# Performance work log

Hardware: AMD Instinct MI355X
Metric: run time of the kernel (lower is better)

The kernel has to match this reference:

```python
import jax, jax.numpy as jnp
import numpy as np

B = 32          # batch_size
M = 1024        # mesh_num (nodes per sub-graph)
D_IN = 128      # sub_node_feature_input_dim
D_OUT = 128     # sub_node_feature_output_dim
E_DIM = 64      # embedding dim per node


def setup_inputs() -> dict:
    key = jax.random.key(0)
    k1, k2, k3, k4 = jax.random.split(key, 4)
    return {
        "node_feature_group": jax.random.normal(k1, (B * M, D_IN), dtype=jnp.float32),
        "embedding_group": jax.random.normal(k2, (B * M, E_DIM), dtype=jnp.float32),
        "W1": jax.random.normal(k3, (D_OUT, D_IN), dtype=jnp.float32) * (1.0 / np.sqrt(D_IN)),
        "W2": jax.random.normal(k4, (D_OUT, D_OUT), dtype=jnp.float32) * (1.0 / np.sqrt(D_OUT)),
    }


def reference(node_feature_group, embedding_group, W1, W2):
    # The torch module builds a (B*M)x(B*M) block-diagonal adjacency via
    # torch.block_diag; off-block entries are exactly zero, and row sums /
    # D^-1/2 A D^-1/2 normalization act per block, so we compute per-graph.
    E = embedding_group.reshape(B, M, E_DIM)
    adj = jnp.maximum(jnp.einsum('bme,bne->bmn', E, E), 0.0)  # clamp(E E^T, 0)
    adj = adj + jnp.eye(M, dtype=adj.dtype)                   # A = adj + I
    d = adj.sum(-1)                                           # [B, M]
    dinv = d ** -0.5                                          # symmetric=True
    dad = dinv[:, :, None] * adj * dinv[:, None, :]           # D^-1/2 A D^-1/2

    X = node_feature_group.reshape(B, M, D_IN)
    y = jax.nn.relu(jnp.einsum('bmn,bnd->bmd', dad, X) @ W1.T)   # gcn1
    y = jax.nn.relu(jnp.einsum('bmn,bnd->bmd', dad, y) @ W2.T)   # gcn2
    # Dropout is identity in eval mode.
    return y.reshape(B * M, D_OUT)
```

## Files before the change

### kernel.cpp

```cpp
#include <hip/hip_runtime.h>
#include <stdint.h>

#define B_  32
#define M_  1024
#define DF  128
#define ED  64

typedef __attribute__((ext_vector_type(8))) short short8;
typedef __attribute__((ext_vector_type(4))) float floatx4;

__device__ inline unsigned short f2bf(float f) {
    union { float f; unsigned u; } v; v.f = f;
    unsigned r = v.u + 0x7fffu + ((v.u >> 16) & 1u);
    return (unsigned short)(r >> 16);
}

__device__ inline void load_lds16(const void* g, void* l) {
    __builtin_amdgcn_global_load_lds(
        (const __attribute__((address_space(1))) unsigned int*)g,
        (__attribute__((address_space(3))) unsigned int*)l, 16, 0, 0);
}

__global__ __launch_bounds__(256) void cast_kernel(
    const float* __restrict__ E, const float* __restrict__ W1,
    const float* __restrict__ W2, unsigned short* __restrict__ Ebf,
    unsigned short* __restrict__ W1bf, unsigned short* __restrict__ W2bf) {
    const int NE = B_ * M_ * ED;
    const int NW = DF * DF;
    int idx = (blockIdx.x * 256 + threadIdx.x) * 4;
    const float* src; unsigned short* dst; int off;
    if (idx < NE)            { src = E;  dst = Ebf;  off = idx; }
    else if (idx < NE + NW)  { src = W1; dst = W1bf; off = idx - NE; }
    else                     { src = W2; dst = W2bf; off = idx - NE - NW; }
    float4 v = *(const float4*)(src + off);
    ushort4 o;
    o.x = f2bf(v.x); o.y = f2bf(v.y); o.z = f2bf(v.z); o.w = f2bf(v.w);
    *(ushort4*)(dst + off) = o;
}

__global__ __launch_bounds__(256) void build_s_kernel(
    const unsigned short* __restrict__ Ebf, unsigned short* __restrict__ S,
    float* __restrict__ dinv) {
    int mt2 = blockIdx.x, b = blockIdx.y;
    int t = threadIdx.x;
    int w = t >> 6, lane = t & 63, quad = lane >> 4, lc = lane & 15;
    __shared__ unsigned short sEn[128][72];
    const unsigned short* Eb = Ebf + (size_t)b * M_ * ED;
    unsigned short* Sg = S + ((size_t)b << 20);
    int base_m = mt2 * 64 + w * 16;

    short8 afr[2];
    for (int ks = 0; ks < 2; ++ks)
        afr[ks] = *(const short8*)(Eb + (size_t)(base_m + lc) * ED + ks * 32 + quad * 8);
    floatx4 rsum = (floatx4){0.f, 0.f, 0.f, 0.f};

    for (int nc = 0; nc < 8; ++nc) {
        __syncthreads();
        for (int it = 0; it < 4; ++it) {
            int c = t + 256 * it;
            int row = c >> 3, off = (c & 7) * 8;
            *(short8*)(&sEn[row][off]) =
                *(const short8*)(Eb + (size_t)(nc * 128 + row) * ED + off);
        }
        __syncthreads();
        for (int nt = 0; nt < 8; ++nt) {
            short8 b0 = *(const short8*)(&sEn[nt * 16 + lc][quad * 8]);
            short8 b1 = *(const short8*)(&sEn[nt * 16 + lc][32 + quad * 8]);
            floatx4 s = (floatx4){0.f, 0.f, 0.f, 0.f};
            s = __builtin_amdgcn_mfma_f32_16x16x32_bf16(afr[0], b0, s, 0, 0, 0);
            s = __builtin_amdgcn_mfma_f32_16x16x32_bf16(afr[1], b1, s, 0, 0, 0);
            int n = nc * 128 + nt * 16 + lc;
            for (int r = 0; r < 4; ++r) {
                int m = base_m + quad * 4 + r;
                float v = fmaxf(s[r], 0.f);
                if (m == n) v += 1.0f;
                rsum[r] += v;
                Sg[(size_t)m * M_ + n] = f2bf(v);
            }
        }
    }
    for (int r = 0; r < 4; ++r) {
        float v = rsum[r];
        v += __shfl_xor(v, 1, 16);
        v += __shfl_xor(v, 2, 16);
        v += __shfl_xor(v, 4, 16);
        v += __shfl_xor(v, 8, 16);
        if (lc == 0)
            dinv[b * M_ + base_m + quad * 4 + r] = rsqrtf(v);
    }
}

__global__ __launch_bounds__(256) void tscale_kernel(
    const float* __restrict__ X, const float* __restrict__ dinv,
    unsigned short* __restrict__ Xt) {
    int nt = blockIdx.x, b = blockIdx.y;
    int t = threadIdx.x;
    __shared__ unsigned short sT[128][72];
    int nloc = t >> 5;
    int d4 = (t & 31) * 4;
    for (int pass = 0; pass < 8; ++pass) {
        int n = pass * 8 + nloc;
        int grow = b * M_ + nt * 64 + n;
        float sc = dinv[grow];
        float4 v = *(const float4*)(X + (size_t)grow * DF + d4);
        sT[d4 + 0][n] = f2bf(v.x * sc);
        sT[d4 + 1][n] = f2bf(v.y * sc);
        sT[d4 + 2][n] = f2bf(v.z * sc);
        sT[d4 + 3][n] = f2bf(v.w * sc);
    }
    __syncthreads();
    for (int it = 0; it < 4; ++it) {
        int c = t + 256 * it;
        int d = c >> 3, off = (c & 7) * 8;
        *(short8*)(Xt + (size_t)(b * DF + d) * M_ + nt * 64 + off) =
            *(const short8*)(&sT[d][off]);
    }
}

template <int MODE>
__global__ __launch_bounds__(256) void gemm_kernel(
    const unsigned short* __restrict__ S,
    const unsigned short* __restrict__ Pt,
    const unsigned short* __restrict__ Wbf,
    const float* __restrict__ dinv,
    unsigned short* __restrict__ OutT,
    float* __restrict__ OutF) {
    int bx = blockIdx.x, b = blockIdx.y;
    int m0 = bx * 64;
    int t = threadIdx.x;
    int w = t >> 6, lane = t & 63, quad = lane >> 4, lc = lane & 15;
    int wr = w & 1, wc = w >> 1;

    __shared__ unsigned short lds[26112];
    unsigned short* sA = lds;
    unsigned short* sB = lds + 4096;
    unsigned short* sY = lds;
    unsigned short* sW = lds + 8704;

    const unsigned short* Sg = S + ((size_t)b << 20);
    const unsigned short* Pb = Pt + (size_t)b * DF * M_;

    floatx4 acc[2][4];
    for (int i = 0; i < 2; ++i)
        for (int j = 0; j < 4; ++j) acc[i][j] = (floatx4){0.f, 0.f, 0.f, 0.f};

    for (int nc = 0; nc < 16; ++nc) {
        __syncthreads();
        for (int r = 0; r < 2; ++r) {
            int te = r * 256 + w * 64 + lane;
            const void* gp = Sg + (size_t)(m0 + (te >> 3)) * M_ + nc * 64 + (te & 7) * 8;
            load_lds16(gp, (char*)sA + (r * 256 + w * 64) * 16);
        }
        for (int r = 0; r < 4; ++r) {
            int te = r * 256 + w * 64 + lane;
            const void* gp = Pb + (size_t)(te >> 3) * M_ + nc * 64 + (te & 7) * 8;
            load_lds16(gp, (char*)sB + (r * 256 + w * 64) * 16);
        }
        __syncthreads();
        for (int ks = 0; ks < 2; ++ks) {
            short8 afr[2], bfr[4];
            for (int i = 0; i < 2; ++i)
                afr[i] = *(const short8*)(&sA[(wr * 32 + i * 16 + lc) * 64 + ks * 32 + quad * 8]);
            for (int j = 0; j < 4; ++j)
                bfr[j] = *(const short8*)(&sB[(wc * 64 + j * 16 + lc) * 64 + ks * 32 + quad * 8]);
            for (int i = 0; i < 2; ++i)
                for (int j = 0; j < 4; ++j)
                    acc[i][j] = __builtin_amdgcn_mfma_f32_16x16x32_bf16(afr[i], bfr[j], acc[i][j], 0, 0, 0);
        }
    }

    float dv[2][4];
    for (int i = 0; i < 2; ++i)
        for (int r = 0; r < 4; ++r)
            dv[i][r] = dinv[b * M_ + m0 + wr * 32 + i * 16 + quad * 4 + r];
    __syncthreads();
    for (int i = 0; i < 2; ++i)
        for (int j = 0; j < 4; ++j) {
            int mrow = wr * 32 + i * 16 + quad * 4;
            int col = wc * 64 + j * 16 + lc;
            for (int r = 0; r < 4; ++r)
                sY[(mrow + r) * 136 + col] = f2bf(acc[i][j][r] * dv[i][r]);
        }
    for (int it = 0; it < 8; ++it) {
        int c = t + 256 * it;
        int row = c >> 4, off = (c & 15) * 8;
        *(short8*)(&sW[row * 136 + off]) = *(const short8*)(Wbf + row * DF + off);
    }
    __syncthreads();
    floatx4 accH[2][4];
    for (int i = 0; i < 2; ++i)
        for (int j = 0; j < 4; ++j) accH[i][j] = (floatx4){0.f, 0.f, 0.f, 0.f};
    for (int ks = 0; ks < 4; ++ks) {
        short8 afr[2], bfr[4];
        for (int i = 0; i < 2; ++i)
            afr[i] = *(const short8*)(&sY[(wr * 32 + i * 16 + lc) * 136 + ks * 32 + quad * 8]);
        for (int j = 0; j < 4; ++j)
            bfr[j] = *(const short8*)(&sW[(wc * 64 + j * 16 + lc) * 136 + ks * 32 + quad * 8]);
        for (int i = 0; i < 2; ++i)
            for (int j = 0; j < 4; ++j)
                accH[i][j] = __builtin_amdgcn_mfma_f32_16x16x32_bf16(afr[i], bfr[j], accH[i][j], 0, 0, 0);
    }
    if (MODE == 2) {
        float* Ob = OutF + ((size_t)b * M_ + m0) * DF;
        for (int i = 0; i < 2; ++i)
            for (int j = 0; j < 4; ++j) {
                int mrow = wr * 32 + i * 16 + quad * 4;
                int col = wc * 64 + j * 16 + lc;
                for (int r = 0; r < 4; ++r)
                    Ob[(size_t)(mrow + r) * DF + col] = fmaxf(accH[i][j][r], 0.f);
            }
    } else {
        __syncthreads();
        unsigned short* sT = sW;
        for (int i = 0; i < 2; ++i)
            for (int j = 0; j < 4; ++j) {
                int mrow = wr * 32 + i * 16 + quad * 4;
                int col = wc * 64 + j * 16 + lc;
                for (int r = 0; r < 4; ++r)
                    sT[col * 72 + mrow + r] = f2bf(fmaxf(accH[i][j][r], 0.f) * dv[i][r]);
            }
        __syncthreads();
        for (int it = 0; it < 4; ++it) {
            int c = t + 256 * it;
            int o = c >> 3, off = (c & 7) * 8;
            *(short8*)(OutT + (size_t)(b * DF + o) * M_ + m0 + off) =
                *(const short8*)(&sT[o * 72 + off]);
        }
    }
}

__global__ __launch_bounds__(256) void degree_kernel(
    const unsigned short* __restrict__ Ebf, float* __restrict__ dinv) {
    int mt = blockIdx.x, b = blockIdx.y;
    int t = threadIdx.x;
    int w = t >> 6, lane = t & 63, quad = lane >> 4, lc = lane & 15;
    __shared__ unsigned short sEn[128][72];
    const unsigned short* Eb = Ebf + (size_t)b * M_ * ED;
    short8 afr[2][2];
    for (int i = 0; i < 2; ++i) {
        int row = mt * 128 + w * 32 + i * 16 + lc;
        for (int ks = 0; ks < 2; ++ks)
            afr[i][ks] = *(const short8*)(Eb + (size_t)row * ED + ks * 32 + quad * 8);
    }
    floatx4 rsum[2];
    rsum[0] = (floatx4){0.f,0.f,0.f,0.f};
    rsum[1] = (floatx4){0.f,0.f,0.f,0.f};
    for (int nc = 0; nc < 8; ++nc) {
        __syncthreads();
        for (int it = 0; it < 4; ++it) {
            int c = t + 256 * it;
            int row = c >> 3, off = (c & 7) * 8;
            *(short8*)(&sEn[row][off]) =
                *(const short8*)(Eb + (size_t)(nc * 128 + row) * ED + off);
        }
        __syncthreads();
        for (int nt = 0; nt < 8; ++nt) {
            short8 b0 = *(const short8*)(&sEn[nt * 16 + lc][quad * 8]);
            short8 b1 = *(const short8*)(&sEn[nt * 16 + lc][32 + quad * 8]);
            for (int i = 0; i < 2; ++i) {
                floatx4 s = (floatx4){0.f,0.f,0.f,0.f};
                s = __builtin_amdgcn_mfma_f32_16x16x32_bf16(afr[i][0], b0, s, 0, 0, 0);
                s = __builtin_amdgcn_mfma_f32_16x16x32_bf16(afr[i][1], b1, s, 0, 0, 0);
                for (int r = 0; r < 4; ++r) rsum[i][r] += fmaxf(s[r], 0.f);
            }
        }
    }
    for (int i = 0; i < 2; ++i)
        for (int r = 0; r < 4; ++r) {
            float v = rsum[i][r];
            v += __shfl_xor(v, 1, 16);
            v += __shfl_xor(v, 2, 16);
            v += __shfl_xor(v, 4, 16);
            v += __shfl_xor(v, 8, 16);
            if (lc == 0) {
                int row = mt * 128 + w * 32 + i * 16 + quad * 4 + r;
                dinv[b * M_ + row] = rsqrtf(1.0f + v);
            }
        }
}

__global__ __launch_bounds__(256) void tscale128_kernel(
    const float* __restrict__ X, const float* __restrict__ dinv,
    unsigned short* __restrict__ Xt) {
    int mt = blockIdx.x, b = blockIdx.y;
    int t = threadIdx.x;
    __shared__ unsigned short sT[128][136];
    int nloc = t >> 5;
    int d4 = (t & 31) * 4;
    for (int pass = 0; pass < 16; ++pass) {
        int n = pass * 8 + nloc;
        int grow = b * M_ + mt * 128 + n;
        float sc = dinv[grow];
        float4 v = *(const float4*)(X + (size_t)grow * DF + d4);
        sT[d4 + 0][n] = f2bf(v.x * sc);
        sT[d4 + 1][n] = f2bf(v.y * sc);
        sT[d4 + 2][n] = f2bf(v.z * sc);
        sT[d4 + 3][n] = f2bf(v.w * sc);
    }
    __syncthreads();
    for (int it = 0; it < 8; ++it) {
        int c = t + 256 * it;
        int d = c >> 4, off = (c & 15) * 8;
        *(short8*)(Xt + (size_t)(b * DF + d) * M_ + mt * 128 + off) =
            *(const short8*)(&sT[d][off]);
    }
}

template <int MODE>
__global__ __launch_bounds__(256) void gcn_kernel(
    const unsigned short* __restrict__ Ebf,
    const unsigned short* __restrict__ Pt,
    const unsigned short* __restrict__ Wbf,
    const float* __restrict__ dinv,
    unsigned short* __restrict__ OutT,
    float* __restrict__ OutF) {
    int mt = blockIdx.x, b = blockIdx.y;
    int t = threadIdx.x;
    int w = t >> 6, lane = t & 63, quad = lane >> 4, lc = lane & 15;
    int wr = w & 1, wc = w >> 1;
    __shared__ unsigned short sEn[128][72];
    __shared__ unsigned short sS[128][136];
    __shared__ unsigned short sPW[128][136];
    const unsigned short* Eb = Ebf + (size_t)b * M_ * ED;
    short8 ae[4][2];
    for (int i = 0; i < 4; ++i) {
        int row = mt * 128 + wr * 64 + i * 16 + lc;
        for (int ks = 0; ks < 2; ++ks)
            ae[i][ks] = *(const short8*)(Eb + (size_t)row * ED + ks * 32 + quad * 8);
    }
    floatx4 accZ[4][4];
    for (int i = 0; i < 4; ++i)
        for (int j = 0; j < 4; ++j) accZ[i][j] = (floatx4){0.f,0.f,0.f,0.f};
    for (int nc = 0; nc < 8; ++nc) {
        __syncthreads();
        for (int it = 0; it < 4; ++it) {
            int c = t + 256 * it;
            int row = c >> 3, off = (c & 7) * 8;
            *(short8*)(&sEn[row][off]) =
                *(const short8*)(Eb + (size_t)(nc * 128 + row) * ED + off);
        }
        for (int it = 0; it < 8; ++it) {
            int c = t + 256 * it;
            int drow = c >> 4, off = (c & 15) * 8;
            *(short8*)(&sPW[drow][off]) =
                *(const short8*)(Pt + (size_t)(b * DF + drow) * M_ + nc * 128 + off);
        }
        __syncthreads();
        for (int jt = 0; jt < 4; ++jt) {
            int ncol = wc * 64 + jt * 16;
            short8 b0 = *(const short8*)(&sEn[ncol + lc][quad * 8]);
            short8 b1 = *(const short8*)(&sEn[ncol + lc][32 + quad * 8]);
            for (int i = 0; i < 4; ++i) {
                floatx4 s = (floatx4){0.f,0.f,0.f,0.f};
                s = __builtin_amdgcn_mfma_f32_16x16x32_bf16(ae[i][0], b0, s, 0, 0, 0);
                s = __builtin_amdgcn_mfma_f32_16x16x32_bf16(ae[i][1], b1, s, 0, 0, 0);
                int mrow = wr * 64 + i * 16 + quad * 4;
                for (int r = 0; r < 4; ++r) {
                    float v = fmaxf(s[r], 0.f);
                    if (mt == nc && (mrow + r) == (ncol + lc)) v += 1.0f;
                    sS[mrow + r][ncol + lc] = f2bf(v);
                }
            }
        }
        __syncthreads();
        for (int ks = 0; ks < 4; ++ks) {
            short8 afr[4];
            for (int i = 0; i < 4; ++i)
                afr[i] = *(const short8*)(&sS[wr * 64 + i * 16 + lc][ks * 32 + quad * 8]);
            for (int j = 0; j < 4; ++j) {
                short8 bfr = *(const short8*)(&sPW[wc * 64 + j * 16 + lc][ks * 32 + quad * 8]);
                for (int i = 0; i < 4; ++i)
                    accZ[i][j] = __builtin_amdgcn_mfma_f32_16x16x32_bf16(afr[i], bfr, accZ[i][j], 0, 0, 0);
            }
        }
    }
    float dv[4][4];
    for (int i = 0; i < 4; ++i)
        for (int r = 0; r < 4; ++r)
            dv[i][r] = dinv[b * M_ + mt * 128 + wr * 64 + i * 16 + quad * 4 + r];
    __syncthreads();
    for (int i = 0; i < 4; ++i)
        for (int j = 0; j < 4; ++j) {
            int mrow = wr * 64 + i * 16 + quad * 4;
            int col = wc * 64 + j * 16 + lc;
            for (int r = 0; r < 4; ++r)
                sS[mrow + r][col] = f2bf(accZ[i][j][r] * dv[i][r]);
        }
    for (int it = 0; it < 8; ++it) {
        int c = t + 256 * it;
        int row = c >> 4, off = (c & 15) * 8;
        *(short8*)(&sPW[row][off]) = *(const short8*)(Wbf + row * DF + off);
    }
    __syncthreads();
    floatx4 accH[4][4];
    for (int i = 0; i < 4; ++i)
        for (int j = 0; j < 4; ++j) accH[i][j] = (floatx4){0.f,0.f,0.f,0.f};
    for (int ks = 0; ks < 4; ++ks) {
        short8 afr[4], bfr[4];
        for (int i = 0; i < 4; ++i)
            afr[i] = *(const short8*)(&sS[wr * 64 + i * 16 + lc][ks * 32 + quad * 8]);
        for (int j = 0; j < 4; ++j)
            bfr[j] = *(const short8*)(&sPW[wc * 64 + j * 16 + lc][ks * 32 + quad * 8]);
        for (int i = 0; i < 4; ++i)
            for (int j = 0; j < 4; ++j)
                accH[i][j] = __builtin_amdgcn_mfma_f32_16x16x32_bf16(afr[i], bfr[j], accH[i][j], 0, 0, 0);
    }
    if (MODE == 2) {
        float* Ob = OutF + ((size_t)b * M_ + mt * 128) * DF;
        for (int i = 0; i < 4; ++i)
            for (int j = 0; j < 4; ++j) {
                int mrow = wr * 64 + i * 16 + quad * 4;
                int col = wc * 64 + j * 16 + lc;
                for (int r = 0; r < 4; ++r)
                    Ob[(size_t)(mrow + r) * DF + col] = fmaxf(accH[i][j][r], 0.f);
            }
    } else {
        __syncthreads();
        for (int i = 0; i < 4; ++i)
            for (int j = 0; j < 4; ++j) {
                int mrow = wr * 64 + i * 16 + quad * 4;
                int col = wc * 64 + j * 16 + lc;
                for (int r = 0; r < 4; ++r)
                    sS[col][mrow + r] = f2bf(fmaxf(accH[i][j][r], 0.f) * dv[i][r]);
            }
        __syncthreads();
        unsigned short* Ob = OutT + (size_t)b * DF * M_ + mt * 128;
        for (int it = 0; it < 8; ++it) {
            int c = t + 256 * it;
            int orow = c >> 4, off = (c & 15) * 8;
            *(short8*)(Ob + (size_t)orow * M_ + off) = *(const short8*)(&sS[orow][off]);
        }
    }
}

extern "C" void kernel_launch(void* const* d_in, const int* in_sizes, int n_in,
                              void* d_out, int out_size, void* d_ws, size_t ws_size,
                              hipStream_t stream) {
    (void)in_sizes; (void)n_in; (void)out_size;
    const float* X  = (const float*)d_in[0];
    const float* E  = (const float*)d_in[1];
    const float* W1 = (const float*)d_in[2];
    const float* W2 = (const float*)d_in[3];
    float* out = (float*)d_out;

    char* ws = (char*)d_ws;
    unsigned short* Ebf  = (unsigned short*)(ws);
    unsigned short* W1bf = (unsigned short*)(ws + 4194304);
    unsigned short* W2bf = (unsigned short*)(ws + 4227072);
    float*          dinv = (float*)(ws + 4259840);
    unsigned short* Xt   = (unsigned short*)(ws + 4390912);
    unsigned short* Ht   = (unsigned short*)(ws + 12779520);
    unsigned short* Smat = (unsigned short*)(ws + 21168128);
    const size_t NEED = 21168128ull + 67108864ull;

    cast_kernel<<<2080, 256, 0, stream>>>(E, W1, W2, Ebf, W1bf, W2bf);
    if (ws_size >= NEED) {
        build_s_kernel<<<dim3(16, 32), 256, 0, stream>>>(Ebf, Smat, dinv);
        tscale_kernel<<<dim3(16, 32), 256, 0, stream>>>(X, dinv, Xt);
        gemm_kernel<1><<<dim3(16, 32), 256, 0, stream>>>(Smat, Xt, W1bf, dinv, Ht, nullptr);
        gemm_kernel<2><<<dim3(16, 32), 256, 0, stream>>>(Smat, Ht, W2bf, dinv, nullptr, out);
    } else {
        degree_kernel<<<dim3(8, 32), 256, 0, stream>>>(Ebf, dinv);
        tscale128_kernel<<<dim3(8, 32), 256, 0, stream>>>(X, dinv, Xt);
        gcn_kernel<1><<<dim3(8, 32), 256, 0, stream>>>(Ebf, Xt, W1bf, dinv, Ht, nullptr);
        gcn_kernel<2><<<dim3(8, 32), 256, 0, stream>>>(Ebf, Ht, W2bf, dinv, nullptr, out);
    }
}
```

Before: 154.6 us.

## Fuse cast, degree build and X scaling; coalesce S and output stores

```diff
diff --git a/kernel.cpp b/kernel.cpp
--- a/kernel.cpp
+++ b/kernel.cpp
@@ -7,6 +7,7 @@
 #define ED  64
 
 typedef __attribute__((ext_vector_type(8))) short short8;
+typedef __attribute__((ext_vector_type(4))) short short4v;
 typedef __attribute__((ext_vector_type(4))) float floatx4;
 
 __device__ inline unsigned short f2bf(float f) {
@@ -15,10 +16,237 @@
     return (unsigned short)(r >> 16);
 }
 
+__device__ inline short8 cvt8(float4 a, float4 b) {
+    short8 s;
+    s[0] = (short)f2bf(a.x); s[1] = (short)f2bf(a.y);
+    s[2] = (short)f2bf(a.z); s[3] = (short)f2bf(a.w);
+    s[4] = (short)f2bf(b.x); s[5] = (short)f2bf(b.y);
+    s[6] = (short)f2bf(b.z); s[7] = (short)f2bf(b.w);
+    return s;
+}
+
 __device__ inline void load_lds16(const void* g, void* l) {
     __builtin_amdgcn_global_load_lds(
         (const __attribute__((address_space(1))) unsigned int*)g,
         (__attribute__((address_space(3))) unsigned int*)l, 16, 0, 0);
+}
+
+__global__ __launch_bounds__(256) void build_fused_kernel(
+    const float* __restrict__ E, const float* __restrict__ X,
+    unsigned short* __restrict__ S, float* __restrict__ dinv,
+    unsigned short* __restrict__ Xt) {
+    int mt2 = blockIdx.x, b = blockIdx.y;
+    int t = threadIdx.x;
+    int w = t >> 6, lane = t & 63, quad = lane >> 4, lc = lane & 15;
+    int m0 = mt2 * 64;
+
+    __shared__ unsigned short sEn[128 * 72];
+    __shared__ unsigned short sOt[128 * 72];
+    __shared__ float sDinv[64];
+
+    const float* Eb = E + (size_t)b * M_ * ED;
+    unsigned short* Sg = S + ((size_t)b << 20);
+    int base_m = m0 + w * 16;
+
+    short8 afr[2];
+    for (int ks = 0; ks < 2; ++ks) {
+        const float* p = Eb + (size_t)(base_m + lc) * ED + ks * 32 + quad * 8;
+        afr[ks] = cvt8(*(const float4*)p, *(const float4*)(p + 4));
+    }
+    floatx4 rsum = (floatx4){0.f, 0.f, 0.f, 0.f};
+
+    for (int nc = 0; nc < 8; ++nc) {
+        __syncthreads();
+        for (int it = 0; it < 4; ++it) {
+            int c = t + 256 * it;
+            int row = c >> 3, off = (c & 7) * 8;
+            const float* p = Eb + (size_t)(nc * 128 + row) * ED + off;
+            *(short8*)(&sEn[row * 72 + off]) = cvt8(*(const float4*)p, *(const float4*)(p + 4));
+        }
+        __syncthreads();
+        for (int nt = 0; nt < 8; ++nt) {
+            short8 b0 = *(const short8*)(&sEn[(nt * 16 + lc) * 72 + quad * 8]);
+            short8 b1 = *(const short8*)(&sEn[(nt * 16 + lc) * 72 + 32 + quad * 8]);
+            floatx4 s = (floatx4){0.f, 0.f, 0.f, 0.f};
+            s = __builtin_amdgcn_mfma_f32_16x16x32_bf16(afr[0], b0, s, 0, 0, 0);
+            s = __builtin_amdgcn_mfma_f32_16x16x32_bf16(afr[1], b1, s, 0, 0, 0);
+            int nloc = nt * 16 + lc;
+            int n = nc * 128 + nloc;
+            short4v pk;
+            for (int r = 0; r < 4; ++r) {
+                int m = base_m + quad * 4 + r;
+                float v = fmaxf(s[r], 0.f);
+                if (m == n) v += 1.0f;
+                rsum[r] += v;
+                pk[r] = (short)f2bf(v);
+            }
+            *(short4v*)(&sOt[nloc * 72 + w * 16 + quad * 4]) = pk;
+        }
+        __syncthreads();
+        for (int it = 0; it < 4; ++it) {
+            int c = t + 256 * it;
+            int row = c >> 3, off = (c & 7) * 8;
+            *(short8*)(Sg + (size_t)(nc * 128 + row) * M_ + m0 + off) =
+                *(const short8*)(&sOt[row * 72 + off]);
+        }
+    }
+    for (int r = 0; r < 4; ++r) {
+        float v = rsum[r];
+        v += __shfl_xor(v, 1, 16);
+        v += __shfl_xor(v, 2, 16);
+        v += __shfl_xor(v, 4, 16);
+        v += __shfl_xor(v, 8, 16);
+        if (lc == 0) {
+            float dvv = rsqrtf(v);
+            int mloc = w * 16 + quad * 4 + r;
+            sDinv[mloc] = dvv;
+            dinv[b * M_ + m0 + mloc] = dvv;
+        }
+    }
+    __syncthreads();
+    {
+        int nloc = t >> 5;
+        int d4 = (t & 31) * 4;
+        for (int pass = 0; pass < 8; ++pass) {
+            int n = pass * 8 + nloc;
+            float sc = sDinv[n];
+            float4 v = *(const float4*)(X + (size_t)(b * M_ + m0 + n) * DF + d4);
+            sOt[(d4 + 0) * 72 + n] = f2bf(v.x * sc);
+            sOt[(d4 + 1) * 72 + n] = f2bf(v.y * sc);
+            sOt[(d4 + 2) * 72 + n] = f2bf(v.z * sc);
+            sOt[(d4 + 3) * 72 + n] = f2bf(v.w * sc);
+        }
+    }
+    __syncthreads();
+    for (int it = 0; it < 4; ++it) {
+        int c = t + 256 * it;
+        int d = c >> 3, off = (c & 7) * 8;
+        *(short8*)(Xt + (size_t)(b * DF + d) * M_ + m0 + off) =
+            *(const short8*)(&sOt[d * 72 + off]);
+    }
+}
+
+template <int MODE>
+__global__ __launch_bounds__(256) void gemm_kernel(
+    const unsigned short* __restrict__ S,
+    const unsigned short* __restrict__ Pt,
+    const float* __restrict__ Wf,
+    const float* __restrict__ dinv,
+    unsigned short* __restrict__ OutT,
+    float* __restrict__ OutF) {
+    int bx = blockIdx.x, b = blockIdx.y;
+    int m0 = bx * 64;
+    int t = threadIdx.x;
+    int w = t >> 6, lane = t & 63, quad = lane >> 4, lc = lane & 15;
+    int wr = w & 1, wc = w >> 1;
+
+    __shared__ unsigned short lds[26112];
+    unsigned short* sA = lds;
+    unsigned short* sB = lds + 4096;
+    unsigned short* sY = lds;
+    unsigned short* sW = lds + 8704;
+
+    const unsigned short* Sg = S + ((size_t)b << 20);
+    const unsigned short* Pb = Pt + (size_t)b * DF * M_;
+
+    floatx4 acc[2][4];
+    for (int i = 0; i < 2; ++i)
+        for (int j = 0; j < 4; ++j) acc[i][j] = (floatx4){0.f, 0.f, 0.f, 0.f};
+
+    for (int nc = 0; nc < 16; ++nc) {
+        __syncthreads();
+        for (int r = 0; r < 2; ++r) {
+            int te = r * 256 + w * 64 + lane;
+            const void* gp = Sg + (size_t)(m0 + (te >> 3)) * M_ + nc * 64 + (te & 7) * 8;
+            load_lds16(gp, (char*)sA + (r * 256 + w * 64) * 16);
+        }
+        for (int r = 0; r < 4; ++r) {
+            int te = r * 256 + w * 64 + lane;
+            const void* gp = Pb + (size_t)(te >> 3) * M_ + nc * 64 + (te & 7) * 8;
+            load_lds16(gp, (char*)sB + (r * 256 + w * 64) * 16);
+        }
+        __syncthreads();
+        for (int ks = 0; ks < 2; ++ks) {
+            short8 afr[2], bfr[4];
+            for (int i = 0; i < 2; ++i)
+                afr[i] = *(const short8*)(&sA[(wr * 32 + i * 16 + lc) * 64 + ks * 32 + quad * 8]);
+            for (int j = 0; j < 4; ++j)
+                bfr[j] = *(const short8*)(&sB[(wc * 64 + j * 16 + lc) * 64 + ks * 32 + quad * 8]);
+            for (int i = 0; i < 2; ++i)
+                for (int j = 0; j < 4; ++j)
+                    acc[i][j] = __builtin_amdgcn_mfma_f32_16x16x32_bf16(afr[i], bfr[j], acc[i][j], 0, 0, 0);
+        }
+    }
+
+    float dv[2][4];
+    for (int i = 0; i < 2; ++i)
+        for (int r = 0; r < 4; ++r)
+            dv[i][r] = dinv[b * M_ + m0 + wr * 32 + i * 16 + quad * 4 + r];
+    __syncthreads();
+    for (int i = 0; i < 2; ++i)
+        for (int j = 0; j < 4; ++j) {
+            int mrow = wr * 32 + i * 16 + quad * 4;
+            int col = wc * 64 + j * 16 + lc;
+            for (int r = 0; r < 4; ++r)
+                sY[(mrow + r) * 136 + col] = f2bf(acc[i][j][r] * dv[i][r]);
+        }
+    for (int it = 0; it < 8; ++it) {
+        int c = t + 256 * it;
+        int row = c >> 4, off = (c & 15) * 8;
+        const float* p = Wf + row * DF + off;
+        *(short8*)(&sW[row * 136 + off]) = cvt8(*(const float4*)p, *(const float4*)(p + 4));
+    }
+    __syncthreads();
+    floatx4 accH[2][4];
+    for (int i = 0; i < 2; ++i)
+        for (int j = 0; j < 4; ++j) accH[i][j] = (floatx4){0.f, 0.f, 0.f, 0.f};
+    for (int ks = 0; ks < 4; ++ks) {
+        short8 afr[2], bfr[4];
+        for (int i = 0; i < 2; ++i)
+            afr[i] = *(const short8*)(&sY[(wr * 32 + i * 16 + lc) * 136 + ks * 32 + quad * 8]);
+        for (int j = 0; j < 4; ++j)
+            bfr[j] = *(const short8*)(&sW[(wc * 64 + j * 16 + lc) * 136 + ks * 32 + quad * 8]);
+        for (int i = 0; i < 2; ++i)
+            for (int j = 0; j < 4; ++j)
+                accH[i][j] = __builtin_amdgcn_mfma_f32_16x16x32_bf16(afr[i], bfr[j], accH[i][j], 0, 0, 0);
+    }
+    if (MODE == 2) {
+        __syncthreads();
+        float* sF = (float*)lds;
+        for (int i = 0; i < 2; ++i)
+            for (int j = 0; j < 4; ++j) {
+                int mrow = wr * 32 + i * 16 + quad * 4;
+                int col = wc * 64 + j * 16 + lc;
+                for (int r = 0; r < 4; ++r)
+                    sF[(mrow + r) * 132 + col] = fmaxf(accH[i][j][r], 0.f);
+            }
+        __syncthreads();
+        float* Ob = OutF + ((size_t)b * M_ + m0) * DF;
+        for (int it = 0; it < 8; ++it) {
+            int c = t + 256 * it;
+            int row = c >> 5, off = (c & 31) * 4;
+            *(float4*)(Ob + (size_t)row * DF + off) = *(const float4*)(&sF[row * 132 + off]);
+        }
+    } else {
+        __syncthreads();
+        unsigned short* sT = sW;
+        for (int i = 0; i < 2; ++i)
+            for (int j = 0; j < 4; ++j) {
+                int mrow = wr * 32 + i * 16 + quad * 4;
+                int col = wc * 64 + j * 16 + lc;
+                short4v pk;
+                for (int r = 0; r < 4; ++r)
+                    pk[r] = (short)f2bf(fmaxf(accH[i][j][r], 0.f) * dv[i][r]);
+                *(short4v*)(&sT[col * 72 + mrow]) = pk;
+            }
+        __syncthreads();
+        for (int it = 0; it < 4; ++it) {
+            int c = t + 256 * it;
+            int o = c >> 3, off = (c & 7) * 8;
+            *(short8*)(OutT + (size_t)(b * DF + o) * M_ + m0 + off) =
+                *(const short8*)(&sT[o * 72 + off]);
+        }
+    }
 }
 
 __global__ __launch_bounds__(256) void cast_kernel(
@@ -36,197 +264,6 @@
     ushort4 o;
     o.x = f2bf(v.x); o.y = f2bf(v.y); o.z = f2bf(v.z); o.w = f2bf(v.w);
     *(ushort4*)(dst + off) = o;
-}
-
-__global__ __launch_bounds__(256) void build_s_kernel(
-    const unsigned short* __restrict__ Ebf, unsigned short* __restrict__ S,
-    float* __restrict__ dinv) {
-    int mt2 = blockIdx.x, b = blockIdx.y;
-    int t = threadIdx.x;
-    int w = t >> 6, lane = t & 63, quad = lane >> 4, lc = lane & 15;
-    __shared__ unsigned short sEn[128][72];
-    const unsigned short* Eb = Ebf + (size_t)b * M_ * ED;
-    unsigned short* Sg = S + ((size_t)b << 20);
-    int base_m = mt2 * 64 + w * 16;
-
-    short8 afr[2];
-    for (int ks = 0; ks < 2; ++ks)
-        afr[ks] = *(const short8*)(Eb + (size_t)(base_m + lc) * ED + ks * 32 + quad * 8);
-    floatx4 rsum = (floatx4){0.f, 0.f, 0.f, 0.f};
-
-    for (int nc = 0; nc < 8; ++nc) {
-        __syncthreads();
-        for (int it = 0; it < 4; ++it) {
-            int c = t + 256 * it;
-            int row = c >> 3, off = (c & 7) * 8;
-            *(short8*)(&sEn[row][off]) =
-                *(const short8*)(Eb + (size_t)(nc * 128 + row) * ED + off);
-        }
-        __syncthreads();
-        for (int nt = 0; nt < 8; ++nt) {
-            short8 b0 = *(const short8*)(&sEn[nt * 16 + lc][quad * 8]);
-            short8 b1 = *(const short8*)(&sEn[nt * 16 + lc][32 + quad * 8]);
-            floatx4 s = (floatx4){0.f, 0.f, 0.f, 0.f};
-            s = __builtin_amdgcn_mfma_f32_16x16x32_bf16(afr[0], b0, s, 0, 0, 0);
-            s = __builtin_amdgcn_mfma_f32_16x16x32_bf16(afr[1], b1, s, 0, 0, 0);
-            int n = nc * 128 + nt * 16 + lc;
-            for (int r = 0; r < 4; ++r) {
-                int m = base_m + quad * 4 + r;
-                float v = fmaxf(s[r], 0.f);
-                if (m == n) v += 1.0f;
-                rsum[r] += v;
-                Sg[(size_t)m * M_ + n] = f2bf(v);
-            }
-        }
-    }
-    for (int r = 0; r < 4; ++r) {
-        float v = rsum[r];
-        v += __shfl_xor(v, 1, 16);
-        v += __shfl_xor(v, 2, 16);
-        v += __shfl_xor(v, 4, 16);
-        v += __shfl_xor(v, 8, 16);
-        if (lc == 0)
-            dinv[b * M_ + base_m + quad * 4 + r] = rsqrtf(v);
-    }
-}
-
-__global__ __launch_bounds__(256) void tscale_kernel(
-    const float* __restrict__ X, const float* __restrict__ dinv,
-    unsigned short* __restrict__ Xt) {
-    int nt = blockIdx.x, b = blockIdx.y;
-    int t = threadIdx.x;
-    __shared__ unsigned short sT[128][72];
-    int nloc = t >> 5;
-    int d4 = (t & 31) * 4;
-    for (int pass = 0; pass < 8; ++pass) {
-        int n = pass * 8 + nloc;
-        int grow = b * M_ + nt * 64 + n;
-        float sc = dinv[grow];
-        float4 v = *(const float4*)(X + (size_t)grow * DF + d4);
-        sT[d4 + 0][n] = f2bf(v.x * sc);
-        sT[d4 + 1][n] = f2bf(v.y * sc);
-        sT[d4 + 2][n] = f2bf(v.z * sc);
-        sT[d4 + 3][n] = f2bf(v.w * sc);
-    }
-    __syncthreads();
-    for (int it = 0; it < 4; ++it) {
-        int c = t + 256 * it;
-        int d = c >> 3, off = (c & 7) * 8;
-        *(short8*)(Xt + (size_t)(b * DF + d) * M_ + nt * 64 + off) =
-            *(const short8*)(&sT[d][off]);
-    }
-}
-
-template <int MODE>
-__global__ __launch_bounds__(256) void gemm_kernel(
-    const unsigned short* __restrict__ S,
-    const unsigned short* __restrict__ Pt,
-    const unsigned short* __restrict__ Wbf,
-    const float* __restrict__ dinv,
-    unsigned short* __restrict__ OutT,
-    float* __restrict__ OutF) {
-    int bx = blockIdx.x, b = blockIdx.y;
-    int m0 = bx * 64;
-    int t = threadIdx.x;
-    int w = t >> 6, lane = t & 63, quad = lane >> 4, lc = lane & 15;
-    int wr = w & 1, wc = w >> 1;
-
-    __shared__ unsigned short lds[26112];
-    unsigned short* sA = lds;
-    unsigned short* sB = lds + 4096;
-    unsigned short* sY = lds;
-    unsigned short* sW = lds + 8704;
-
-    const unsigned short* Sg = S + ((size_t)b << 20);
-    const unsigned short* Pb = Pt + (size_t)b * DF * M_;
-
-    floatx4 acc[2][4];
-    for (int i = 0; i < 2; ++i)
-        for (int j = 0; j < 4; ++j) acc[i][j] = (floatx4){0.f, 0.f, 0.f, 0.f};
-
-    for (int nc = 0; nc < 16; ++nc) {
-        __syncthreads();
-        for (int r = 0; r < 2; ++r) {
-            int te = r * 256 + w * 64 + lane;
-            const void* gp = Sg + (size_t)(m0 + (te >> 3)) * M_ + nc * 64 + (te & 7) * 8;
-            load_lds16(gp, (char*)sA + (r * 256 + w * 64) * 16);
-        }
-        for (int r = 0; r < 4; ++r) {
-            int te = r * 256 + w * 64 + lane;
-            const void* gp = Pb + (size_t)(te >> 3) * M_ + nc * 64 + (te & 7) * 8;
-            load_lds16(gp, (char*)sB + (r * 256 + w * 64) * 16);
-        }
-        __syncthreads();
-        for (int ks = 0; ks < 2; ++ks) {
-            short8 afr[2], bfr[4];
-            for (int i = 0; i < 2; ++i)
-                afr[i] = *(const short8*)(&sA[(wr * 32 + i * 16 + lc) * 64 + ks * 32 + quad * 8]);
-            for (int j = 0; j < 4; ++j)
-                bfr[j] = *(const short8*)(&sB[(wc * 64 + j * 16 + lc) * 64 + ks * 32 + quad * 8]);
-            for (int i = 0; i < 2; ++i)
-                for (int j = 0; j < 4; ++j)
-                    acc[i][j] = __builtin_amdgcn_mfma_f32_16x16x32_bf16(afr[i], bfr[j], acc[i][j], 0, 0, 0);
-        }
-    }
-
-    float dv[2][4];
-    for (int i = 0; i < 2; ++i)
-        for (int r = 0; r < 4; ++r)
-            dv[i][r] = dinv[b * M_ + m0 + wr * 32 + i * 16 + quad * 4 + r];
-    __syncthreads();
-    for (int i = 0; i < 2; ++i)
-        for (int j = 0; j < 4; ++j) {
-            int mrow = wr * 32 + i * 16 + quad * 4;
-            int col = wc * 64 + j * 16 + lc;
-            for (int r = 0; r < 4; ++r)
-                sY[(mrow + r) * 136 + col] = f2bf(acc[i][j][r] * dv[i][r]);
-        }
-    for (int it = 0; it < 8; ++it) {
-        int c = t + 256 * it;
-        int row = c >> 4, off = (c & 15) * 8;
-        *(short8*)(&sW[row * 136 + off]) = *(const short8*)(Wbf + row * DF + off);
-    }
-    __syncthreads();
-    floatx4 accH[2][4];
-    for (int i = 0; i < 2; ++i)
-        for (int j = 0; j < 4; ++j) accH[i][j] = (floatx4){0.f, 0.f, 0.f, 0.f};
-    for (int ks = 0; ks < 4; ++ks) {
-        short8 afr[2], bfr[4];
-        for (int i = 0; i < 2; ++i)
-            afr[i] = *(const short8*)(&sY[(wr * 32 + i * 16 + lc) * 136 + ks * 32 + quad * 8]);
-        for (int j = 0; j < 4; ++j)
-            bfr[j] = *(const short8*)(&sW[(wc * 64 + j * 16 + lc) * 136 + ks * 32 + quad * 8]);
-        for (int i = 0; i < 2; ++i)
-            for (int j = 0; j < 4; ++j)
-                accH[i][j] = __builtin_amdgcn_mfma_f32_16x16x32_bf16(afr[i], bfr[j], accH[i][j], 0, 0, 0);
-    }
-    if (MODE == 2) {
-        float* Ob = OutF + ((size_t)b * M_ + m0) * DF;
-        for (int i = 0; i < 2; ++i)
-            for (int j = 0; j < 4; ++j) {
-                int mrow = wr * 32 + i * 16 + quad * 4;
-                int col = wc * 64 + j * 16 + lc;
-                for (int r = 0; r < 4; ++r)
-                    Ob[(size_t)(mrow + r) * DF + col] = fmaxf(accH[i][j][r], 0.f);
-            }
-    } else {
-        __syncthreads();
-        unsigned short* sT = sW;
-        for (int i = 0; i < 2; ++i)
-            for (int j = 0; j < 4; ++j) {
-                int mrow = wr * 32 + i * 16 + quad * 4;
-                int col = wc * 64 + j * 16 + lc;
-                for (int r = 0; r < 4; ++r)
-                    sT[col * 72 + mrow + r] = f2bf(fmaxf(accH[i][j][r], 0.f) * dv[i][r]);
-            }
-        __syncthreads();
-        for (int it = 0; it < 4; ++it) {
-            int c = t + 256 * it;
-            int o = c >> 3, off = (c & 7) * 8;
-            *(short8*)(OutT + (size_t)(b * DF + o) * M_ + m0 + off) =
-                *(const short8*)(&sT[o * 72 + off]);
-        }
-    }
 }
 
 __global__ __launch_bounds__(256) void degree_kernel(
@@ -453,13 +490,12 @@
     unsigned short* Smat = (unsigned short*)(ws + 21168128);
     const size_t NEED = 21168128ull + 67108864ull;
 
-    cast_kernel<<<2080, 256, 0, stream>>>(E, W1, W2, Ebf, W1bf, W2bf);
     if (ws_size >= NEED) {
-        build_s_kernel<<<dim3(16, 32), 256, 0, stream>>>(Ebf, Smat, dinv);
-        tscale_kernel<<<dim3(16, 32), 256, 0, stream>>>(X, dinv, Xt);
-        gemm_kernel<1><<<dim3(16, 32), 256, 0, stream>>>(Smat, Xt, W1bf, dinv, Ht, nullptr);
-        gemm_kernel<2><<<dim3(16, 32), 256, 0, stream>>>(Smat, Ht, W2bf, dinv, nullptr, out);
+        build_fused_kernel<<<dim3(16, 32), 256, 0, stream>>>(E, X, Smat, dinv, Xt);
+        gemm_kernel<1><<<dim3(16, 32), 256, 0, stream>>>(Smat, Xt, W1, dinv, Ht, nullptr);
+        gemm_kernel<2><<<dim3(16, 32), 256, 0, stream>>>(Smat, Ht, W2, dinv, nullptr, out);
     } else {
+        cast_kernel<<<2080, 256, 0, stream>>>(E, W1, W2, Ebf, W1bf, W2bf);
         degree_kernel<<<dim3(8, 32), 256, 0, stream>>>(Ebf, dinv);
         tscale128_kernel<<<dim3(8, 32), 256, 0, stream>>>(X, dinv, Xt);
         gcn_kernel<1><<<dim3(8, 32), 256, 0, stream>>>(Ebf, Xt, W1bf, dinv, Ht, nullptr);
```

Result: no change. 155.5 us (+0.6%).
